# Optimization experiments

Hardware: AMD Instinct MI355X
Metric: run time of the kernel (lower is better)

The kernel has to match this reference:

```python
import jax, jax.numpy as jnp
import numpy as np

B, N, C, H, I, ID = 4, 1024, 1024, 16, 77, 768
HD = C // H
HID = 4 * C


def _ln(t, w, b):
    m = jnp.mean(t, axis=-1, keepdims=True)
    v = jnp.mean((t - m) ** 2, axis=-1, keepdims=True)
    return (t - m) * jax.lax.rsqrt(v + 1e-5) * w + b


def _gelu(t):
    return jax.nn.gelu(t, approximate=False)


def setup_inputs() -> dict:
    key = jax.random.key(0)
    ks = iter(jax.random.split(key, 16))

    def nrm(shape, s=0.02):
        return jax.random.normal(next(ks), shape, jnp.float32) * s

    return {
        'x': jax.random.normal(next(ks), (B, N, C), jnp.float32),
        'instruct_states': jax.random.normal(next(ks), (B, I, ID), jnp.float32),
        'norm1_w': jnp.ones((C,), jnp.float32), 'norm1_b': jnp.zeros((C,), jnp.float32),
        'qkv_w': nrm((3 * C, C)),
        'q_bias': jnp.zeros((C,), jnp.float32), 'v_bias': jnp.zeros((C,), jnp.float32),
        'proj_w': nrm((C, C)), 'proj_b': jnp.zeros((C,), jnp.float32),
        'gamma_1': jnp.full((C,), 1e-5, jnp.float32), 'gamma_2': jnp.full((C,), 1e-5, jnp.float32),
        'norm2_w': jnp.ones((C,), jnp.float32), 'norm2_b': jnp.zeros((C,), jnp.float32),
        'fc1_w': nrm((HID, C)), 'fc1_b': jnp.zeros((HID,), jnp.float32),
        'fc2_w': nrm((C, HID)), 'fc2_b': jnp.zeros((C,), jnp.float32),
        'pfc1_w': nrm((HID, C)), 'pfc1_b': jnp.zeros((HID,), jnp.float32),
        'pfc2_w': nrm((C, HID)), 'pfc2_b': jnp.zeros((C,), jnp.float32),
        'parallel_gate': jnp.full((1,), 0.1, jnp.float32),
        'ir_ln_w': jnp.ones((ID,), jnp.float32), 'ir_ln_b': jnp.zeros((ID,), jnp.float32),
        'ir_l1_w': nrm((C, ID)), 'ir_l1_b': jnp.zeros((C,), jnp.float32),
        'ir_l2_w': nrm((C, C)), 'ir_l2_b': jnp.zeros((C,), jnp.float32),
    }


def reference(x, instruct_states, norm1_w, norm1_b, qkv_w, q_bias, v_bias,
              proj_w, proj_b, gamma_1, gamma_2, norm2_w, norm2_b,
              fc1_w, fc1_b, fc2_w, fc2_b, pfc1_w, pfc1_b, pfc2_w, pfc2_b,
              parallel_gate, ir_ln_w, ir_ln_b, ir_l1_w, ir_l1_b, ir_l2_w, ir_l2_b):
    # instruct_dim_reduce: LN -> Linear -> GELU -> Linear
    kv = _ln(instruct_states, ir_ln_w, ir_ln_b)
    kv = _gelu(kv @ ir_l1_w.T + ir_l1_b) @ ir_l2_w.T + ir_l2_b  # [B, I, C]

    xn = _ln(x, norm1_w, norm1_b)                               # [B, N, C]
    cat = jnp.concatenate([kv, xn], axis=1)                     # [B, I+N, C]
    S = I + N

    qkv_bias = jnp.concatenate([q_bias, jnp.zeros_like(v_bias), v_bias])
    qkv = (cat @ qkv_w.T + qkv_bias).reshape(B, S, 3, H, HD)
    q = qkv[:, :, 0].transpose(0, 2, 1, 3)                      # [B, H, S, HD]
    k = qkv[:, :, 1].transpose(0, 2, 1, 3)
    v = qkv[:, :, 2].transpose(0, 2, 1, 3)

    # only visual queries, keys/values over instructions + visual tokens
    q = q[:, :, I:, :] * (HD ** -0.5)                           # [B, H, N, HD]
    attn = jnp.einsum('bhqd,bhkd->bhqk', q, k)                  # [B, H, N, S]
    attn = jax.nn.softmax(attn, axis=-1)
    o = jnp.einsum('bhqk,bhkd->bqhd', attn, v).reshape(B, N, C)
    o = o @ proj_w.T + proj_b

    x = x + gamma_1 * o                                         # LayerScale residual

    y = _ln(x, norm2_w, norm2_b)
    mlp = _gelu(y @ fc1_w.T + fc1_b) @ fc2_w.T + fc2_b
    pmlp = _gelu(y @ pfc1_w.T + pfc1_b) @ pfc2_w.T + pfc2_b
    x = x + gamma_2 * mlp + parallel_gate * pmlp
    return x
```

## Files before the change

kernel.cpp:

```cpp
#include <hip/hip_runtime.h>
#include <cstdint>

#define Bv   4
#define Nv   1024
#define Cv   1024
#define Hv   16
#define Iv   77
#define IDv  768
#define HDv  64
#define HIDv 4096
#define Sv   (Iv + Nv)
#define BIv  (Bv * Iv)
#define BSv  (Bv * Sv)
#define BNv  (Bv * Nv)
#define SPADv 1152

typedef __bf16 bf16x8_t __attribute__((ext_vector_type(8)));
typedef float  f32x4_t  __attribute__((ext_vector_type(4)));
typedef unsigned short us8_t __attribute__((ext_vector_type(8)));
typedef long  l2_t  __attribute__((ext_vector_type(2)));
typedef int   i32x4_t __attribute__((ext_vector_type(4)));
typedef int   i32x8_t __attribute__((ext_vector_type(8)));

__device__ inline f32x4_t zero4() { f32x4_t z; z[0]=0.f; z[1]=0.f; z[2]=0.f; z[3]=0.f; return z; }

__device__ inline unsigned short f2bf(float f) {
    unsigned int u = __builtin_bit_cast(unsigned int, f);
    u = (u + 0x7fffu + ((u >> 16) & 1u)) >> 16;
    return (unsigned short)u;
}
__device__ inline float bf2f(unsigned short u) {
    return __builtin_bit_cast(float, ((unsigned int)u) << 16);
}
__device__ inline unsigned int f4_fp8(float a, float b, float c, float d) {
    int v = __builtin_amdgcn_cvt_pk_fp8_f32(a, b, 0, false);
    v = __builtin_amdgcn_cvt_pk_fp8_f32(c, d, v, true);
    return (unsigned int)v;
}

__device__ inline float gelu_f(float x) {
    float u = 0.7978845608f * x * (1.0f + 0.044715f * x * x);
    float e = __expf(2.0f * u);
    float t = 1.0f - 2.0f / (e + 1.0f);
    return 0.5f * x * (1.0f + t);
}

__device__ inline void gload_lds16(const void* g, void* l) {
    __builtin_amdgcn_global_load_lds(
        (__attribute__((address_space(1))) void*)(unsigned long long)g,
        (__attribute__((address_space(3))) void*)(unsigned long long)l,
        16, 0, 0);
}

__device__ inline i32x8_t frag32(const unsigned char* p0, const unsigned char* p1) {
    i32x4_t lo = *(const i32x4_t*)p0;
    i32x4_t hi = *(const i32x4_t*)p1;
    i32x8_t r;
    r[0] = lo[0]; r[1] = lo[1]; r[2] = lo[2]; r[3] = lo[3];
    r[4] = hi[0]; r[5] = hi[1]; r[6] = hi[2]; r[7] = hi[3];
    return r;
}

#define PIPE_WAIT(N) do { \
    asm volatile("s_waitcnt vmcnt(" #N ")" ::: "memory"); \
    __builtin_amdgcn_s_barrier(); \
    __builtin_amdgcn_sched_barrier(0); \
} while (0)
#define PIPE_RELEASE() do { \
    __builtin_amdgcn_sched_barrier(0); \
    __builtin_amdgcn_s_barrier(); \
} while (0)

__global__ __launch_bounds__(256) void cvt8_kernel(
        const float* s0, const float* s1, const float* s2, const float* s3,
        const float* s4, const float* s5, const float* s6, const float* s7,
        void* d0, void* d1, void* d2, void* d3,
        void* d4, void* d5, void* d6, void* d7,
        const float* g1, const float* g2, const float* gate) {
    (void)g1;
    long i = (long)blockIdx.x * 256 + threadIdx.x;
    const float* src; void* dst; long off;
    const float* sptr = nullptr; int K4 = 1; float wmul = 1.0f; bool f8 = false;
    if (i < 2097152) {
        if (i < 786432)       { src = s0; dst = d0; off = i; f8 = true; wmul = 32.f; }
        else if (i < 1048576) { src = s1; dst = d1; off = i - 786432;  f8 = true; wmul = 32.f; }
        else                  { src = s2; dst = d2; off = i - 1048576; f8 = true; wmul = 32.f; }
    } else if (i < 4194304) {
        if (i < 3145728)      { src = s3; dst = d3; off = i - 2097152; f8 = true; wmul = 32.f; sptr = g2; K4 = 1024; }
        else                  { src = s4; dst = d4; off = i - 3145728; f8 = true; wmul = 32.f; }
    } else {
        if (i < 5242880)      { src = s5; dst = d5; off = i - 4194304; f8 = true; wmul = 32.f; sptr = gate; K4 = 0x7fffffff; }
        else if (i < 5439488) { src = s6; dst = d6; off = i - 5242880; }
        else                  { src = s7; dst = d7; off = i - 5439488; }
    }
    float sc = (sptr ? sptr[(int)(off / K4)] : 1.0f) * wmul;
    float4 v = ((const float4*)src)[off];
    if (f8) {
        ((unsigned int*)dst)[off] = f4_fp8(v.x * sc, v.y * sc, v.z * sc, v.w * sc);
    } else {
        ushort4 o = {f2bf(v.x * sc), f2bf(v.y * sc), f2bf(v.z * sc), f2bf(v.w * sc)};
        ((ushort4*)dst)[off] = o;
    }
}

__global__ __launch_bounds__(256) void bias_prep_kernel(
        const float* __restrict__ qb, const float* __restrict__ vb,
        const float* __restrict__ fc2b, const float* __restrict__ pfc2b,
        const float* __restrict__ projb_in,
        const float* __restrict__ fc1b, const float* __restrict__ pfc1b,
        const float* __restrict__ g1, const float* __restrict__ g2,
        const float* __restrict__ gate,
        float* __restrict__ qkvb, float* __restrict__ bfuse,
        float* __restrict__ projb, float* __restrict__ bcat) {
    int i = blockIdx.x * 256 + threadIdx.x;
    if (i < 3 * Cv) {
        float v = 0.f;
        if (i < Cv) v = qb[i];
        else if (i >= 2 * Cv) v = vb[i - 2 * Cv];
        qkvb[i] = v;
    } else if (i < 4 * Cv) {
        int n = i - 3 * Cv;
        bfuse[n] = g2[n] * fc2b[n] + gate[0] * pfc2b[n];
    } else if (i < 5 * Cv) {
        int n = i - 4 * Cv;
        projb[n] = g1[n] * projb_in[n];
    } else if (i < 13 * Cv) {
        int j = i - 5 * Cv;
        bcat[j] = (j < HIDv) ? fc1b[j] : pfc1b[j - HIDv];
    }
}

template <int F8>
__global__ __launch_bounds__(256) void ln_kernel(const float* __restrict__ in,
                                                 const float* __restrict__ w,
                                                 const float* __restrict__ bvec,
                                                 void* __restrict__ out,
                                                 int cols, float invcols,
                                                 int div_, int stride_, int off_) {
    const int r = blockIdx.x;
    const int tid = threadIdx.x;
    const float* row = in + (size_t)r * cols;
    float s = 0.f, s2 = 0.f;
    for (int c = tid * 4; c < cols; c += 1024) {
        float4 v = *(const float4*)(row + c);
        s  += v.x + v.y + v.z + v.w;
        s2 += v.x * v.x + v.y * v.y + v.z * v.z + v.w * v.w;
    }
#pragma unroll
    for (int o2 = 32; o2 > 0; o2 >>= 1) { s += __shfl_down(s, o2); s2 += __shfl_down(s2, o2); }
    __shared__ float sh[10];
    const int lane = tid & 63, wave = tid >> 6;
    if (lane == 0) { sh[wave] = s; sh[4 + wave] = s2; }
    __syncthreads();
    if (tid == 0) {
        float S1 = sh[0] + sh[1] + sh[2] + sh[3];
        float S2 = sh[4] + sh[5] + sh[6] + sh[7];
        float mean = S1 * invcols;
        float var  = S2 * invcols - mean * mean;
        sh[8] = mean;
        sh[9] = rsqrtf(var + 1e-5f);
    }
    __syncthreads();
    const float mean = sh[8], rstd = sh[9];
    const size_t orow = (size_t)((r / div_) * stride_ + (r % div_) + off_) * cols;
    for (int c = tid * 4; c < cols; c += 1024) {
        float4 v  = *(const float4*)(row + c);
        float4 wv = *(const float4*)(w + c);
        float4 bv = *(const float4*)(bvec + c);
        float o0 = (v.x - mean) * rstd * wv.x + bv.x;
        float o1 = (v.y - mean) * rstd * wv.y + bv.y;
        float o2 = (v.z - mean) * rstd * wv.z + bv.z;
        float o3 = (v.w - mean) * rstd * wv.w + bv.w;
        if constexpr (F8) {
            *(unsigned int*)((unsigned char*)out + orow + c) =
                f4_fp8(o0 * 16.f, o1 * 16.f, o2 * 16.f, o3 * 16.f);
        } else {
            ushort4 o = {f2bf(o0), f2bf(o1), f2bf(o2), f2bf(o3)};
            *(ushort4*)((unsigned short*)out + orow + c) = o;
        }
    }
}

__global__ __launch_bounds__(256) void proj_ln2_kernel(
        const unsigned short* __restrict__ parts,
        const float* __restrict__ x,
        const float* __restrict__ projb,
        const float* __restrict__ g1,
        const float* __restrict__ w, const float* __restrict__ bvec,
        float* __restrict__ x1, unsigned char* __restrict__ y8) {
    const int r = blockIdx.x;
    const int tid = threadIdx.x;
    const int c = tid * 4;
    const size_t base = (size_t)r * Cv + c;
    float4 xv = *(const float4*)(x + base);
    float4 pb = *(const float4*)(projb + c);
    float4 gv = *(const float4*)(g1 + c);
    ushort4 u0 = *(const ushort4*)(parts + base);
    ushort4 u1 = *(const ushort4*)(parts + (size_t)BNv * Cv + base);
    float4 v;
    v.x = xv.x + pb.x + gv.x * (bf2f(u0.x) + bf2f(u1.x));
    v.y = xv.y + pb.y + gv.y * (bf2f(u0.y) + bf2f(u1.y));
    v.z = xv.z + pb.z + gv.z * (bf2f(u0.z) + bf2f(u1.z));
    v.w = xv.w + pb.w + gv.w * (bf2f(u0.w) + bf2f(u1.w));
    *(float4*)(x1 + base) = v;

    float s  = v.x + v.y + v.z + v.w;
    float s2 = v.x * v.x + v.y * v.y + v.z * v.z + v.w * v.w;
#pragma unroll
    for (int o2 = 32; o2 > 0; o2 >>= 1) { s += __shfl_down(s, o2); s2 += __shfl_down(s2, o2); }
    __shared__ float sh[10];
    const int lane = tid & 63, wave = tid >> 6;
    if (lane == 0) { sh[wave] = s; sh[4 + wave] = s2; }
    __syncthreads();
    if (tid == 0) {
        float S1 = sh[0] + sh[1] + sh[2] + sh[3];
        float S2 = sh[4] + sh[5] + sh[6] + sh[7];
        float mean = S1 * (1.0f / Cv);
        float var  = S2 * (1.0f / Cv) - mean * mean;
        sh[8] = mean;
        sh[9] = rsqrtf(var + 1e-5f);
    }
    __syncthreads();
    const float mean = sh[8], rstd = sh[9];
    float4 wv = *(const float4*)(w + c);
    float4 bv = *(const float4*)(bvec + c);
    float o0 = (v.x - mean) * rstd * wv.x + bv.x;
    float o1 = (v.y - mean) * rstd * wv.y + bv.y;
    float o2 = (v.z - mean) * rstd * wv.z + bv.z;
    float o3 = (v.w - mean) * rstd * wv.w + bv.w;
    *(unsigned int*)(y8 + base) = f4_fp8(o0 * 16.f, o1 * 16.f, o2 * 16.f, o3 * 16.f);
}

template <int MODE>
__global__ __launch_bounds__(256) void gemm_bf16_kernel(
        const unsigned short* __restrict__ A,
        const unsigned short* __restrict__ W,
        const float* __restrict__ bias,
        unsigned short* __restrict__ outp,
        int M, int N, int K) {
    __shared__ unsigned short As[2][128 * 32];
    __shared__ unsigned short Bs[2][128 * 32];
    const int tid  = threadIdx.x;
    const int lane = tid & 63;
    const int wave = tid >> 6;
    const int m16  = lane & 15;
    const int g4   = lane >> 4;
    const int n0 = blockIdx.x * 128;
    const int m0 = blockIdx.y * 128;
    const int wm = (wave >> 1) * 64;
    const int wn = (wave & 1) * 64;

    const int r0  = tid >> 2;
    const int cc0 = (tid & 3) * 8;
    int am0 = m0 + r0;       if (am0 > M - 1) am0 = M - 1;
    int am1 = m0 + r0 + 64;  if (am1 > M - 1) am1 = M - 1;
    const unsigned short* agp0 = A + (size_t)am0 * K + cc0;
    const unsigned short* agp1 = A + (size_t)am1 * K + cc0;
    const unsigned short* bgp0 = W + (size_t)(n0 + r0) * K + cc0;
    const unsigned short* bgp1 = W + (size_t)(n0 + r0 + 64) * K + cc0;

    f32x4_t acc[4][4];
#pragma unroll
    for (int a = 0; a < 4; ++a)
#pragma unroll
        for (int bb = 0; bb < 4; ++bb) acc[a][bb] = zero4();

    auto stage = [&](int buf) {
        gload_lds16(agp0, &As[buf][wave * 512]);
        gload_lds16(agp1, &As[buf][2048 + wave * 512]);
        gload_lds16(bgp0, &Bs[buf][wave * 512]);
        gload_lds16(bgp1, &Bs[buf][2048 + wave * 512]);
        agp0 += 32; agp1 += 32; bgp0 += 32; bgp1 += 32;
    };

    auto body = [&](int cur) {
        bf16x8_t xf[4], wf[4];
#pragma unroll
        for (int bb = 0; bb < 4; ++bb)
            xf[bb] = *(const bf16x8_t*)&As[cur][(wm + bb * 16 + m16) * 32 + g4 * 8];
#pragma unroll
        for (int a = 0; a < 4; ++a)
            wf[a] = *(const bf16x8_t*)&Bs[cur][(wn + a * 16 + m16) * 32 + g4 * 8];
#pragma unroll
        for (int a = 0; a < 4; ++a)
#pragma unroll
            for (int bb = 0; bb < 4; ++bb)
                acc[a][bb] = __builtin_amdgcn_mfma_f32_16x16x32_bf16(wf[a], xf[bb], acc[a][bb], 0, 0, 0);
    };

    const int NIT = K >> 5;
    stage(0);
    stage(1);
    for (int it = 0; it < NIT - 1; ++it) {
        const int cur = it & 1;
        PIPE_WAIT(4);
        body(cur);
        PIPE_RELEASE();
        if (it + 2 < NIT) stage(cur);
    }
    PIPE_WAIT(0);
    body((NIT - 1) & 1);

#pragma unroll
    for (int a = 0; a < 4; ++a) {
        const int cb = n0 + wn + a * 16 + g4 * 4;
        const float4 bv4 = *(const float4*)(bias + cb);
#pragma unroll
        for (int bb = 0; bb < 4; ++bb) {
            const int r = m0 + wm + bb * 16 + m16;
            if (r < M) {
                const float v0 = acc[a][bb][0] + bv4.x;
                const float v1 = acc[a][bb][1] + bv4.y;
                const float v2 = acc[a][bb][2] + bv4.z;
                const float v3 = acc[a][bb][3] + bv4.w;
                if constexpr (MODE == 0) {
                    const size_t idx = (size_t)r * N + cb;
                    ushort4 o = {f2bf(v0), f2bf(v1), f2bf(v2), f2bf(v3)};
                    *(ushort4*)(outp + idx) = o;
                } else if constexpr (MODE == 1) {
                    const size_t idx = (size_t)r * N + cb;
                    ushort4 o = {f2bf(gelu_f(v0)), f2bf(gelu_f(v1)),
                                 f2bf(gelu_f(v2)), f2bf(gelu_f(v3))};
                    *(ushort4*)(outp + idx) = o;
                } else {
                    const int rr2 = (r / Iv) * Sv + (r % Iv);
                    *(unsigned int*)((unsigned char*)outp + (size_t)rr2 * Cv + cb) =
                        f4_fp8(v0 * 16.f, v1 * 16.f, v2 * 16.f, v3 * 16.f);
                }
            }
        }
    }
}

__global__ __launch_bounds__(256) void gemm_fp8_bf16out_kernel(
        const unsigned char* __restrict__ A,
        const unsigned char* __restrict__ W,
        const float* __restrict__ bias,
        unsigned short* __restrict__ outp,
        int M, int N, int K) {
    __shared__ unsigned char As[2][128 * 128];
    __shared__ unsigned char Bs[2][128 * 128];
    const int tid  = threadIdx.x;
    const int lane = tid & 63;
    const int wave = tid >> 6;
    const int m16  = lane & 15;
    const int g4   = lane >> 4;
    const int n0 = blockIdx.x * 128;
    const int m0 = blockIdx.y * 128;
    const int wm = (wave >> 1) * 64;
    const int wn = (wave & 1) * 64;

    const int rowin = tid >> 3;
    const int sslot = (tid & 7) ^ (rowin & 7);
    const unsigned char* agp[4];
#pragma unroll
    for (int j = 0; j < 4; ++j) {
        int gr = m0 + j * 32 + rowin; if (gr > M - 1) gr = M - 1;
        agp[j] = A + (size_t)gr * K + sslot * 16;
    }
    const unsigned char* bgp = W + (size_t)(n0 + rowin) * K + sslot * 16;

    const int sw = m16 & 7;
    const int ra0 = ((2 * g4) ^ sw) * 16;
    const int ra1 = ((2 * g4 + 1) ^ sw) * 16;

    f32x4_t acc[4][4];
#pragma unroll
    for (int a = 0; a < 4; ++a)
#pragma unroll
        for (int bb = 0; bb < 4; ++bb) acc[a][bb] = zero4();

    auto stage = [&](int buf) {
#pragma unroll
        for (int j = 0; j < 4; ++j) {
            gload_lds16(agp[j], &As[buf][j * 4096 + wave * 1024]);
            gload_lds16(bgp + (size_t)j * 32 * K, &Bs[buf][j * 4096 + wave * 1024]);
            agp[j] += 128;
        }
        bgp += 128;
    };

    stage(0);
    const int NIT = K >> 7;
    for (int it = 0; it < NIT; ++it) {
        const int cur = it & 1;
        __syncthreads();
        if (it + 1 < NIT) stage(cur ^ 1);
        i32x8_t xv[4], wv[4];
#pragma unroll
        for (int bb = 0; bb < 4; ++bb) {
            const unsigned char* rb = &As[cur][(wm + bb * 16 + m16) * 128];
            xv[bb] = frag32(rb + ra0, rb + ra1);
        }
#pragma unroll
        for (int a = 0; a < 4; ++a) {
            const unsigned char* rb = &Bs[cur][(wn + a * 16 + m16) * 128];
            wv[a] = frag32(rb + ra0, rb + ra1);
        }
#pragma unroll
        for (int a = 0; a < 4; ++a)
#pragma unroll
            for (int bb = 0; bb < 4; ++bb)
                acc[a][bb] = __builtin_amdgcn_mfma_scale_f32_16x16x128_f8f6f4(
                    wv[a], xv[bb], acc[a][bb], 0, 0, 0, 0x7f7f7f7f, 0, 0x7f7f7f7f);
    }

    const float ds = 1.0f / 512.0f;
#pragma unroll
    for (int a = 0; a < 4; ++a) {
        const int cb = n0 + wn + a * 16 + g4 * 4;
        const float4 bv4 = *(const float4*)(bias + cb);
#pragma unroll
        for (int bb = 0; bb < 4; ++bb) {
            const int r = m0 + wm + bb * 16 + m16;
            if (r < M) {
                const size_t idx = (size_t)r * N + cb;
                ushort4 o = {f2bf(acc[a][bb][0] * ds + bv4.x),
                             f2bf(acc[a][bb][1] * ds + bv4.y),
                             f2bf(acc[a][bb][2] * ds + bv4.z),
                             f2bf(acc[a][bb][3] * ds + bv4.w)};
                *(ushort4*)(outp + idx) = o;
            }
        }
    }
}

__global__ __launch_bounds__(256) void gemm_fp8_gelu_kernel(
        const unsigned char* __restrict__ A,
        const unsigned char* __restrict__ W,
        const float* __restrict__ bias,
        unsigned char* __restrict__ outp,
        int M, int N, int K) {
    __shared__ unsigned char As[2][128 * 128];
    __shared__ unsigned char Bs[2][128 * 128];
    const int tid  = threadIdx.x;
    const int lane = tid & 63;
    const int wave = tid >> 6;
    const int m16  = lane & 15;
    const int g4   = lane >> 4;
    const int bid = blockIdx.x;
    const int xcd = bid & 7, l = bid >> 3;
    const int by = (xcd << 2) | (l & 3);
    const int bx = l >> 2;
    const int n0 = bx * 128;
    const int m0 = by * 128;
    const int wm = (wave >> 1) * 64;
    const int wn = (wave & 1) * 64;

    const int rowin = tid >> 3;
    const int sslot = (tid & 7) ^ (rowin & 7);
    const unsigned char* agp = A + (size_t)(m0 + rowin) * K + sslot * 16;
    const unsigned char* bgp = W + (size_t)(n0 + rowin) * K + sslot * 16;

    const int sw = m16 & 7;
    const int ra0 = ((2 * g4) ^ sw) * 16;
    const int ra1 = ((2 * g4 + 1) ^ sw) * 16;

    f32x4_t acc[4][4];
#pragma unroll
    for (int a = 0; a < 4; ++a)
#pragma unroll
        for (int bb = 0; bb < 4; ++bb) acc[a][bb] = zero4();

    auto stage = [&](int buf) {
#pragma unroll
        for (int j = 0; j < 4; ++j) {
            gload_lds16(agp + (size_t)j * 32 * K, &As[buf][j * 4096 + wave * 1024]);
            gload_lds16(bgp + (size_t)j * 32 * K, &Bs[buf][j * 4096 + wave * 1024]);
        }
        agp += 128; bgp += 128;
    };

    stage(0);
    const int NIT = K >> 7;
    for (int it = 0; it < NIT; ++it) {
        const int cur = it & 1;
        __syncthreads();
        if (it + 1 < NIT) stage(cur ^ 1);
        i32x8_t xv[4], wv[4];
#pragma unroll
        for (int bb = 0; bb < 4; ++bb) {
            const unsigned char* rb = &As[cur][(wm + bb * 16 + m16) * 128];
            xv[bb] = frag32(rb + ra0, rb + ra1);
        }
#pragma unroll
        for (int a = 0; a < 4; ++a) {
            const unsigned char* rb = &Bs[cur][(wn + a * 16 + m16) * 128];
            wv[a] = frag32(rb + ra0, rb + ra1);
        }
#pragma unroll
        for (int a = 0; a < 4; ++a)
#pragma unroll
            for (int bb = 0; bb < 4; ++bb)
                acc[a][bb] = __builtin_amdgcn_mfma_scale_f32_16x16x128_f8f6f4(
                    wv[a], xv[bb], acc[a][bb], 0, 0, 0, 0x7f7f7f7f, 0, 0x7f7f7f7f);
    }

    const float ds = 1.0f / 512.0f;
#pragma unroll
    for (int a = 0; a < 4; ++a) {
        const int cb = n0 + wn + a * 16 + g4 * 4;
        const float4 bv4 = *(const float4*)(bias + cb);
#pragma unroll
        for (int bb = 0; bb < 4; ++bb) {
            const int r = m0 + wm + bb * 16 + m16;
            const size_t idx = (size_t)r * N + cb;
            unsigned int pk = f4_fp8(gelu_f(acc[a][bb][0] * ds + bv4.x) * 16.f,
                                     gelu_f(acc[a][bb][1] * ds + bv4.y) * 16.f,
                                     gelu_f(acc[a][bb][2] * ds + bv4.z) * 16.f,
                                     gelu_f(acc[a][bb][3] * ds + bv4.w) * 16.f);
            *(unsigned int*)(outp + idx) = pk;
        }
    }
}

__global__ __launch_bounds__(256) void gemm_fp8_splitk_kernel(
        const unsigned char* __restrict__ A1,
        const unsigned char* __restrict__ W1,
        const unsigned char* __restrict__ A2,
        const unsigned char* __restrict__ W2,
        unsigned short* __restrict__ parts,
        int M, int N, int lda, int ldw, int Kc, int zsplit) {
    __shared__ unsigned char As[2][128 * 128];
    __shared__ unsigned char Bs[2][128 * 128];
    const int tid  = threadIdx.x;
    const int lane = tid & 63;
    const int wave = tid >> 6;
    const int m16  = lane & 15;
    const int g4   = lane >> 4;
    const int bid = blockIdx.x;
    const int xcd = bid & 7, l = bid >> 3;
    const int by = (xcd << 2) | (l & 3);
    const int rr = l >> 2;
    const int bx = rr & 7;
    const int z  = rr >> 3;
    const int n0 = bx * 128;
    const int m0 = by * 128;
    const int wm = (wave >> 1) * 64;
    const int wn = (wave & 1) * 64;

    const unsigned char* A = (z < zsplit) ? A1 : A2;
    const unsigned char* W = (z < zsplit) ? W1 : W2;
    const int k0 = (z % zsplit) * Kc;

    const int rowin = tid >> 3;
    const int sslot = (tid & 7) ^ (rowin & 7);
    const unsigned char* agp = A + (size_t)(m0 + rowin) * lda + k0 + sslot * 16;
    const unsigned char* bgp = W + (size_t)(n0 + rowin) * ldw + k0 + sslot * 16;

    const int sw = m16 & 7;
    const int ra0 = ((2 * g4) ^ sw) * 16;
    const int ra1 = ((2 * g4 + 1) ^ sw) * 16;

    f32x4_t acc[4][4];
#pragma unroll
    for (int a = 0; a < 4; ++a)
#pragma unroll
        for (int bb = 0; bb < 4; ++bb) acc[a][bb] = zero4();

    auto stage = [&](int buf) {
#pragma unroll
        for (int j = 0; j < 4; ++j) {
            gload_lds16(agp + (size_t)j * 32 * lda, &As[buf][j * 4096 + wave * 1024]);
            gload_lds16(bgp + (size_t)j * 32 * ldw, &Bs[buf][j * 4096 + wave * 1024]);
        }
        agp += 128; bgp += 128;
    };

    stage(0);
    const int NIT = Kc >> 7;
    for (int it = 0; it < NIT; ++it) {
        const int cur = it & 1;
        __syncthreads();
        if (it + 1 < NIT) stage(cur ^ 1);
        i32x8_t xv[4], wv[4];
#pragma unroll
        for (int bb = 0; bb < 4; ++bb) {
            const unsigned char* rb = &As[cur][(wm + bb * 16 + m16) * 128];
            xv[bb] = frag32(rb + ra0, rb + ra1);
        }
#pragma unroll
        for (int a = 0; a < 4; ++a) {
            const unsigned char* rb = &Bs[cur][(wn + a * 16 + m16) * 128];
            wv[a] = frag32(rb + ra0, rb + ra1);
        }
#pragma unroll
        for (int a = 0; a < 4; ++a)
#pragma unroll
            for (int bb = 0; bb < 4; ++bb)
                acc[a][bb] = __builtin_amdgcn_mfma_scale_f32_16x16x128_f8f6f4(
                    wv[a], xv[bb], acc[a][bb], 0, 0, 0, 0x7f7f7f7f, 0, 0x7f7f7f7f);
    }

    unsigned short* pz = parts + (size_t)z * M * N;
    const float ds = 1.0f / 512.0f;
#pragma unroll
    for (int a = 0; a < 4; ++a) {
        const int cb = n0 + wn + a * 16 + g4 * 4;
#pragma unroll
        for (int bb = 0; bb < 4; ++bb) {
            const int r = m0 + wm + bb * 16 + m16;
            const size_t idx = (size_t)r * N + cb;
            ushort4 o = {f2bf(acc[a][bb][0] * ds), f2bf(acc[a][bb][1] * ds),
                         f2bf(acc[a][bb][2] * ds), f2bf(acc[a][bb][3] * ds)};
            *(ushort4*)(pz + idx) = o;
        }
    }
}

template <int NP>
__global__ __launch_bounds__(256) void reduce_kernel(
        const unsigned short* __restrict__ parts,
        const float* __restrict__ resid,
        const float* __restrict__ bias,
        float* __restrict__ out, int MN, int N4mask) {
    int i = blockIdx.x * 256 + threadIdx.x;
    if (i * 4 >= MN) return;
    float4 res = ((const float4*)resid)[i];
    float4 bv  = *(const float4*)(bias + (i & N4mask) * 4);
    float4 o = {res.x + bv.x, res.y + bv.y, res.z + bv.z, res.w + bv.w};
#pragma unroll
    for (int z = 0; z < NP; ++z) {
        ushort4 u = ((const ushort4*)(parts + (size_t)z * MN))[i];
        o.x += bf2f(u.x); o.y += bf2f(u.y); o.z += bf2f(u.z); o.w += bf2f(u.w);
    }
    ((float4*)out)[i] = o;
}

__global__ __launch_bounds__(256) void vtrans_kernel(const unsigned short* __restrict__ qkv,
                                                     unsigned short* __restrict__ vt) {
    __shared__ unsigned short Vs[64 * 64];
    const int stile = blockIdx.x;
    const int bh = blockIdx.y;
    const int b = bh >> 4, h = bh & 15;
    const int tid = threadIdx.x;
#pragma unroll
    for (int j = 0; j < 2; ++j) {
        int c = j * 256 + tid;
        int r = c >> 3, d8 = (c & 7) * 8;
        int s = stile * 64 + r;
        uint4 v = {0u, 0u, 0u, 0u};
        if (s < Sv) v = *(const uint4*)(qkv + ((size_t)(b * Sv + s) * 3 + 2) * Cv + h * 64 + d8);
        *(uint4*)&Vs[r * 64 + d8] = v;
    }
    __syncthreads();
    const int d  = tid >> 2;
    const int p0 = (tid & 3) * 16;
    unsigned short tmp[16];
#pragma unroll
    for (int e = 0; e < 16; ++e) {
        int p = p0 + e;
        int s_local = (p & 32) + 16 * ((p >> 2) & 1) + 4 * ((p & 31) >> 3) + (p & 3);
        tmp[e] = Vs[s_local * 64 + d];
    }
    unsigned short* dst = vt + ((size_t)bh * 64 + d) * SPADv + stile * 64 + p0;
    *(uint4*)dst       = *(const uint4*)&tmp[0];
    *(uint4*)(dst + 8) = *(const uint4*)&tmp[8];
}

__global__ __launch_bounds__(256) void attn_kernel(const unsigned short* __restrict__ qkv,
                                                   const unsigned short* __restrict__ vt,
                                                   unsigned char* __restrict__ o) {
    __shared__ unsigned short Qs[64 * 64];
    __shared__ unsigned short Ks[2][64 * 64];
    __shared__ unsigned short Vts[2][64 * 64];

    const int tid  = threadIdx.x;
    const int lane = tid & 63;
    const int wave = tid >> 6;
    const int m16  = lane & 15;
    const int g4   = lane >> 4;
    const int qt = blockIdx.x;
    const int bh = blockIdx.y;
    const int b = bh >> 4, h = bh & 15;

    const int lr = lane >> 3;
    const int csw = ((lane & 7) ^ lr) * 8;
    const int sw7 = m16 & 7;

#pragma unroll
    for (int j = 0; j < 2; ++j) {
        int r = wave * 16 + j * 8 + lr;
        int s = Iv + qt * 64 + r;
        gload_lds16(qkv + ((size_t)(b * Sv + s) * 3) * Cv + h * 64 + csw,
                    &Qs[(wave * 16 + j * 8) * 64]);
    }

    auto stage_kv = [&](int st, int buf) {
#pragma unroll
        for (int j = 0; j < 2; ++j) {
            int r = wave * 16 + j * 8 + lr;
            int s = st * 64 + r; if (s > Sv - 1) s = Sv - 1;
            gload_lds16(qkv + ((size_t)(b * Sv + s) * 3 + 1) * Cv + h * 64 + csw,
                        &Ks[buf][(wave * 16 + j * 8) * 64]);
            gload_lds16(vt + ((size_t)bh * 64 + r) * SPADv + st * 64 + csw,
                        &Vts[buf][(wave * 16 + j * 8) * 64]);
        }
    };

    f32x4_t oacc[4];
#pragma unroll
    for (int dt = 0; dt < 4; ++dt) oacc[dt] = zero4();
    float m_run = -1e30f, l_run = 0.f;

    stage_kv(0, 0);
    __syncthreads();

    const bf16x8_t qf0 = *(const bf16x8_t*)&Qs[(wave * 16 + m16) * 64 + ((g4 ^ sw7) * 8)];
    const bf16x8_t qf1 = *(const bf16x8_t*)&Qs[(wave * 16 + m16) * 64 + (((4 + g4) ^ sw7) * 8)];

    const int NT = (Sv + 63) / 64;
    for (int st = 0; st < NT; ++st) {
        const int cur = st & 1;
        if (st + 1 < NT) stage_kv(st + 1, cur ^ 1);

        f32x4_t sc[4];
#pragma unroll
        for (int kt = 0; kt < 4; ++kt) {
            bf16x8_t k0 = *(const bf16x8_t*)&Ks[cur][(kt * 16 + m16) * 64 + ((g4 ^ sw7) * 8)];
            bf16x8_t k1 = *(const bf16x8_t*)&Ks[cur][(kt * 16 + m16) * 64 + (((4 + g4) ^ sw7) * 8)];
            f32x4_t z = zero4();
            z = __builtin_amdgcn_mfma_f32_16x16x32_bf16(k0, qf0, z, 0, 0, 0);
            z = __builtin_amdgcn_mfma_f32_16x16x32_bf16(k1, qf1, z, 0, 0, 0);
            sc[kt] = z;
        }

        float mx = -1e30f;
#pragma unroll
        for (int kt = 0; kt < 4; ++kt)
#pragma unroll
            for (int r = 0; r < 4; ++r) {
                int key = st * 64 + kt * 16 + g4 * 4 + r;
                float v = sc[kt][r] * 0.125f;
                v = (key < Sv) ? v : -1e30f;
                sc[kt][r] = v;
                mx = fmaxf(mx, v);
            }
        mx = fmaxf(mx, __shfl_xor(mx, 16));
        mx = fmaxf(mx, __shfl_xor(mx, 32));
        const float mnew  = fmaxf(m_run, mx);
        const float alpha = __expf(m_run - mnew);
        m_run = mnew;
        float sum = 0.f;
#pragma unroll
        for (int kt = 0; kt < 4; ++kt)
#pragma unroll
            for (int r = 0; r < 4; ++r) {
                float p = __expf(sc[kt][r] - mnew);
                sc[kt][r] = p;
                sum += p;
            }
        sum += __shfl_xor(sum, 16);
        sum += __shfl_xor(sum, 32);
        l_run = l_run * alpha + sum;
#pragma unroll
        for (int dt = 0; dt < 4; ++dt) oacc[dt] *= alpha;

        us8_t pu0, pu1;
#pragma unroll
        for (int j = 0; j < 8; ++j) {
            pu0[j] = f2bf(sc[(j >> 2)][j & 3]);
            pu1[j] = f2bf(sc[2 + (j >> 2)][j & 3]);
        }
        const bf16x8_t pf0 = __builtin_bit_cast(bf16x8_t, pu0);
        const bf16x8_t pf1 = __builtin_bit_cast(bf16x8_t, pu1);

#pragma unroll
        for (int dt = 0; dt < 4; ++dt) {
            bf16x8_t v0 = *(const bf16x8_t*)&Vts[cur][(dt * 16 + m16) * 64 + ((g4 ^ sw7) * 8)];
            bf16x8_t v1 = *(const bf16x8_t*)&Vts[cur][(dt * 16 + m16) * 64 + (((4 + g4) ^ sw7) * 8)];
            oacc[dt] = __builtin_amdgcn_mfma_f32_16x16x32_bf16(v0, pf0, oacc[dt], 0, 0, 0);
            oacc[dt] = __builtin_amdgcn_mfma_f32_16x16x32_bf16(v1, pf1, oacc[dt], 0, 0, 0);
        }
        __syncthreads();
    }

    const float inv16 = 16.0f / l_run;
    const int q = qt * 64 + wave * 16 + m16;
    const size_t row = (size_t)(b * Nv + q) * Cv + h * 64;
#pragma unroll
    for (int dt = 0; dt < 4; ++dt) {
        *(unsigned int*)&o[row + dt * 16 + g4 * 4] =
            f4_fp8(oacc[dt][0] * inv16, oacc[dt][1] * inv16,
                   oacc[dt][2] * inv16, oacc[dt][3] * inv16);
    }
}

extern "C" void kernel_launch(void* const* d_in, const int* in_sizes, int n_in,
                              void* d_out, int out_size, void* d_ws, size_t ws_size,
                              hipStream_t stream) {
    (void)in_sizes; (void)n_in; (void)out_size; (void)ws_size;
    const float* x       = (const float*)d_in[0];
    const float* instr   = (const float*)d_in[1];
    const float* norm1_w = (const float*)d_in[2];
    const float* norm1_b = (const float*)d_in[3];
    const float* qkv_w   = (const float*)d_in[4];
    const float* q_bias  = (const float*)d_in[5];
    const float* v_bias  = (const float*)d_in[6];
    const float* proj_w  = (const float*)d_in[7];
    const float* proj_b  = (const float*)d_in[8];
    const float* gamma_1 = (const float*)d_in[9];
    const float* gamma_2 = (const float*)d_in[10];
    const float* norm2_w = (const float*)d_in[11];
    const float* norm2_b = (const float*)d_in[12];
    const float* fc1_w   = (const float*)d_in[13];
    const float* fc1_b   = (const float*)d_in[14];
    const float* fc2_w   = (const float*)d_in[15];
    const float* fc2_b   = (const float*)d_in[16];
    const float* pfc1_w  = (const float*)d_in[17];
    const float* pfc1_b  = (const float*)d_in[18];
    const float* pfc2_w  = (const float*)d_in[19];
    const float* pfc2_b  = (const float*)d_in[20];
    const float* gate    = (const float*)d_in[21];
    const float* ir_ln_w = (const float*)d_in[22];
    const float* ir_ln_b = (const float*)d_in[23];
    const float* ir_l1_w = (const float*)d_in[24];
    const float* ir_l1_b = (const float*)d_in[25];
    const float* ir_l2_w = (const float*)d_in[26];
    const float* ir_l2_b = (const float*)d_in[27];
    float* out = (float*)d_out;

    char* ws = (char*)d_ws;
    size_t off = 0;
    auto alloc = [&](size_t bytes) -> char* {
        char* p = ws + off;
        off += (bytes + 255) & ~(size_t)255;
        return p;
    };
    unsigned char*  w_qkv8 = (unsigned char*)alloc((size_t)3 * Cv * Cv);
    unsigned char*  w_proj8= (unsigned char*)alloc((size_t)Cv * Cv);
    unsigned char*  w_mlp1 = (unsigned char*)alloc((size_t)2 * HIDv * Cv);
    unsigned char*  w_fc2  = (unsigned char*)alloc((size_t)Cv * HIDv);
    unsigned char*  w_pfc2 = (unsigned char*)alloc((size_t)Cv * HIDv);
    unsigned short* w_ir1  = (unsigned short*)alloc((size_t)Cv * IDv * 2);
    unsigned short* w_ir2  = (unsigned short*)alloc((size_t)Cv * Cv * 2);
    float*          qkvb   = (float*)alloc((size_t)3 * Cv * 4);
    float*          bfuse  = (float*)alloc((size_t)Cv * 4);
    float*          projb  = (float*)alloc((size_t)Cv * 4);
    float*          bcat   = (float*)alloc((size_t)2 * HIDv * 4);
    unsigned short* irln   = (unsigned short*)alloc((size_t)BIv * IDv * 2);
    unsigned short* h1     = (unsigned short*)alloc((size_t)BIv * Cv * 2);
    unsigned char*  cat8   = (unsigned char*)alloc((size_t)BSv * Cv);
    unsigned short* qkvbuf = (unsigned short*)alloc((size_t)BSv * 3 * Cv * 2);
    unsigned char*  obuf8  = (unsigned char*)alloc((size_t)BNv * Cv);
    float*          x1     = (float*)alloc((size_t)BNv * Cv * 4);
    unsigned char*  ybuf8  = (unsigned char*)alloc((size_t)BNv * Cv);
    unsigned char*  gbufA  = (unsigned char*)alloc((size_t)BNv * 2 * HIDv);
    unsigned short* fpart  = (unsigned short*)alloc((size_t)2 * BNv * Cv * 2);
    unsigned short* vt     = (unsigned short*)gbufA;
    unsigned short* ppart  = fpart;

    cvt8_kernel<<<22272, 256, 0, stream>>>(qkv_w, proj_w, fc1_w, fc2_w, pfc1_w, pfc2_w,
                                           ir_l1_w, ir_l2_w,
                                           w_qkv8, w_proj8, w_mlp1, w_fc2,
                                           w_mlp1 + (size_t)HIDv * Cv, w_pfc2,
                                           w_ir1, w_ir2,
                                           gamma_1, gamma_2, gate);

    bias_prep_kernel<<<52, 256, 0, stream>>>(q_bias, v_bias, fc2_b, pfc2_b, proj_b,
                                             fc1_b, pfc1_b,
                                             gamma_1, gamma_2, gate,
                                             qkvb, bfuse, projb, bcat);

    ln_kernel<0><<<BIv, 256, 0, stream>>>(instr, ir_ln_w, ir_ln_b, irln,
                                          IDv, 1.0f / IDv, 1 << 28, 0, 0);
    ln_kernel<1><<<BNv, 256, 0, stream>>>(x, norm1_w, norm1_b, cat8,
                                          Cv, 1.0f / Cv, Nv, Sv, Iv);
    gemm_bf16_kernel<1><<<dim3(Cv / 128, (BIv + 127) / 128), 256, 0, stream>>>(
        irln, w_ir1, ir_l1_b, h1, BIv, Cv, IDv);
    gemm_bf16_kernel<2><<<dim3(Cv / 128, (BIv + 127) / 128), 256, 0, stream>>>(
        h1, w_ir2, ir_l2_b, (unsigned short*)cat8, BIv, Cv, Cv);

    gemm_fp8_bf16out_kernel<<<dim3(3 * Cv / 128, (BSv + 127) / 128), 256, 0, stream>>>(
        cat8, w_qkv8, qkvb, qkvbuf, BSv, 3 * Cv, Cv);

    vtrans_kernel<<<dim3(18, Bv * Hv), 256, 0, stream>>>(qkvbuf, vt);
    attn_kernel<<<dim3(Nv / 64, Bv * Hv), 256, 0, stream>>>(qkvbuf, vt, obuf8);

    gemm_fp8_splitk_kernel<<<512, 256, 0, stream>>>(
        obuf8, w_proj8, obuf8, w_proj8, ppart,
        BNv, Cv, Cv, Cv, Cv / 2, 2);
    proj_ln2_kernel<<<BNv, 256, 0, stream>>>(
        ppart, x, projb, gamma_1, norm2_w, norm2_b, x1, ybuf8);

    gemm_fp8_gelu_kernel<<<2048, 256, 0, stream>>>(
        ybuf8, w_mlp1, bcat, gbufA, BNv, 2 * HIDv, Cv);

    gemm_fp8_splitk_kernel<<<512, 256, 0, stream>>>(
        gbufA, w_fc2, gbufA + HIDv, w_pfc2, fpart,
        BNv, Cv, 2 * HIDv, HIDv, HIDv, 1);
    reduce_kernel<2><<<(BNv * Cv / 4 + 255) / 256, 256, 0, stream>>>(
        fpart, x1, bfuse, out, BNv * Cv, Cv / 4 - 1);
}
```

Measured before the change: 438.7 us.

## Replace instruct-reduce GEMMs with per-wave tiny tiles; raise MFMA priority in attention

The two small instruction-reduction GEMMs (M=308) now use a kernel where each wave computes a 16x64 tile, loading operands straight from global memory with no LDS staging or barriers. This gives far more blocks than the old 128x128 tiling, which launched only 24 blocks, so it is meant to spread the small problem across more CUs. The trade is no data reuse through shared memory. Separately, the attention kernel raises wave priority around its MFMA sections with s_setprio, to interleave compute better with the softmax and loads of other waves.

```diff
diff --git a/kernel.cpp b/kernel.cpp
--- a/kernel.cpp
+++ b/kernel.cpp
@@ -60,16 +60,6 @@
     r[4] = hi[0]; r[5] = hi[1]; r[6] = hi[2]; r[7] = hi[3];
     return r;
 }
-
-#define PIPE_WAIT(N) do { \
-    asm volatile("s_waitcnt vmcnt(" #N ")" ::: "memory"); \
-    __builtin_amdgcn_s_barrier(); \
-    __builtin_amdgcn_sched_barrier(0); \
-} while (0)
-#define PIPE_RELEASE() do { \
-    __builtin_amdgcn_sched_barrier(0); \
-    __builtin_amdgcn_s_barrier(); \
-} while (0)
 
 __global__ __launch_bounds__(256) void cvt8_kernel(
         const float* s0, const float* s1, const float* s2, const float* s3,
@@ -232,102 +222,59 @@
 }
 
 template <int MODE>
-__global__ __launch_bounds__(256) void gemm_bf16_kernel(
+__global__ __launch_bounds__(256) void gemm_tiny_kernel(
         const unsigned short* __restrict__ A,
         const unsigned short* __restrict__ W,
         const float* __restrict__ bias,
         unsigned short* __restrict__ outp,
         int M, int N, int K) {
-    __shared__ unsigned short As[2][128 * 32];
-    __shared__ unsigned short Bs[2][128 * 32];
-    const int tid  = threadIdx.x;
-    const int lane = tid & 63;
-    const int wave = tid >> 6;
+    const int lane = threadIdx.x & 63;
+    const int wave = threadIdx.x >> 6;
     const int m16  = lane & 15;
     const int g4   = lane >> 4;
-    const int n0 = blockIdx.x * 128;
-    const int m0 = blockIdx.y * 128;
-    const int wm = (wave >> 1) * 64;
-    const int wn = (wave & 1) * 64;
-
-    const int r0  = tid >> 2;
-    const int cc0 = (tid & 3) * 8;
-    int am0 = m0 + r0;       if (am0 > M - 1) am0 = M - 1;
-    int am1 = m0 + r0 + 64;  if (am1 > M - 1) am1 = M - 1;
-    const unsigned short* agp0 = A + (size_t)am0 * K + cc0;
-    const unsigned short* agp1 = A + (size_t)am1 * K + cc0;
-    const unsigned short* bgp0 = W + (size_t)(n0 + r0) * K + cc0;
-    const unsigned short* bgp1 = W + (size_t)(n0 + r0 + 64) * K + cc0;
-
-    f32x4_t acc[4][4];
-#pragma unroll
-    for (int a = 0; a < 4; ++a)
-#pragma unroll
-        for (int bb = 0; bb < 4; ++bb) acc[a][bb] = zero4();
-
-    auto stage = [&](int buf) {
-        gload_lds16(agp0, &As[buf][wave * 512]);
-        gload_lds16(agp1, &As[buf][2048 + wave * 512]);
-        gload_lds16(bgp0, &Bs[buf][wave * 512]);
-        gload_lds16(bgp1, &Bs[buf][2048 + wave * 512]);
-        agp0 += 32; agp1 += 32; bgp0 += 32; bgp1 += 32;
-    };
-
-    auto body = [&](int cur) {
-        bf16x8_t xf[4], wf[4];
-#pragma unroll
-        for (int bb = 0; bb < 4; ++bb)
-            xf[bb] = *(const bf16x8_t*)&As[cur][(wm + bb * 16 + m16) * 32 + g4 * 8];
-#pragma unroll
-        for (int a = 0; a < 4; ++a)
-            wf[a] = *(const bf16x8_t*)&Bs[cur][(wn + a * 16 + m16) * 32 + g4 * 8];
-#pragma unroll
-        for (int a = 0; a < 4; ++a)
-#pragma unroll
-            for (int bb = 0; bb < 4; ++bb)
-                acc[a][bb] = __builtin_amdgcn_mfma_f32_16x16x32_bf16(wf[a], xf[bb], acc[a][bb], 0, 0, 0);
-    };
-
-    const int NIT = K >> 5;
-    stage(0);
-    stage(1);
-    for (int it = 0; it < NIT - 1; ++it) {
-        const int cur = it & 1;
-        PIPE_WAIT(4);
-        body(cur);
-        PIPE_RELEASE();
-        if (it + 2 < NIT) stage(cur);
-    }
-    PIPE_WAIT(0);
-    body((NIT - 1) & 1);
-
+    const int wid  = blockIdx.x * 4 + wave;
+    const int ntiles = N >> 6;
+    const int mti = wid / ntiles;
+    if (mti * 16 >= M + 15) return;
+    const int m0 = mti * 16;
+    const int n0 = (wid % ntiles) * 64;
+
+    int am = m0 + m16; if (am > M - 1) am = M - 1;
+    const unsigned short* ap = A + (size_t)am * K + g4 * 8;
+    const unsigned short* wp = W + (size_t)(n0 + m16) * K + g4 * 8;
+
+    f32x4_t acc[4];
+#pragma unroll
+    for (int a = 0; a < 4; ++a) acc[a] = zero4();
+
+#pragma unroll 2
+    for (int kk = 0; kk < K; kk += 32) {
+        bf16x8_t xf = *(const bf16x8_t*)(ap + kk);
+#pragma unroll
+        for (int a = 0; a < 4; ++a) {
+            bf16x8_t wf = *(const bf16x8_t*)(wp + (size_t)a * 16 * K + kk);
+            acc[a] = __builtin_amdgcn_mfma_f32_16x16x32_bf16(wf, xf, acc[a], 0, 0, 0);
+        }
+    }
+
+    const int r = m0 + m16;
+    if (r >= M) return;
 #pragma unroll
     for (int a = 0; a < 4; ++a) {
-        const int cb = n0 + wn + a * 16 + g4 * 4;
+        const int cb = n0 + a * 16 + g4 * 4;
         const float4 bv4 = *(const float4*)(bias + cb);
-#pragma unroll
-        for (int bb = 0; bb < 4; ++bb) {
-            const int r = m0 + wm + bb * 16 + m16;
-            if (r < M) {
-                const float v0 = acc[a][bb][0] + bv4.x;
-                const float v1 = acc[a][bb][1] + bv4.y;
-                const float v2 = acc[a][bb][2] + bv4.z;
-                const float v3 = acc[a][bb][3] + bv4.w;
-                if constexpr (MODE == 0) {
-                    const size_t idx = (size_t)r * N + cb;
-                    ushort4 o = {f2bf(v0), f2bf(v1), f2bf(v2), f2bf(v3)};
-                    *(ushort4*)(outp + idx) = o;
-                } else if constexpr (MODE == 1) {
-                    const size_t idx = (size_t)r * N + cb;
-                    ushort4 o = {f2bf(gelu_f(v0)), f2bf(gelu_f(v1)),
-                                 f2bf(gelu_f(v2)), f2bf(gelu_f(v3))};
-                    *(ushort4*)(outp + idx) = o;
-                } else {
-                    const int rr2 = (r / Iv) * Sv + (r % Iv);
-                    *(unsigned int*)((unsigned char*)outp + (size_t)rr2 * Cv + cb) =
-                        f4_fp8(v0 * 16.f, v1 * 16.f, v2 * 16.f, v3 * 16.f);
-                }
-            }
+        const float v0 = acc[a][0] + bv4.x;
+        const float v1 = acc[a][1] + bv4.y;
+        const float v2 = acc[a][2] + bv4.z;
+        const float v3 = acc[a][3] + bv4.w;
+        if constexpr (MODE == 1) {
+            ushort4 o = {f2bf(gelu_f(v0)), f2bf(gelu_f(v1)),
+                         f2bf(gelu_f(v2)), f2bf(gelu_f(v3))};
+            *(ushort4*)(outp + (size_t)r * N + cb) = o;
+        } else {
+            const int rr2 = (r / Iv) * Sv + (r % Iv);
+            *(unsigned int*)((unsigned char*)outp + (size_t)rr2 * Cv + cb) =
+                f4_fp8(v0 * 16.f, v1 * 16.f, v2 * 16.f, v3 * 16.f);
         }
     }
 }
@@ -715,6 +662,7 @@
         if (st + 1 < NT) stage_kv(st + 1, cur ^ 1);
 
         f32x4_t sc[4];
+        __builtin_amdgcn_s_setprio(1);
 #pragma unroll
         for (int kt = 0; kt < 4; ++kt) {
             bf16x8_t k0 = *(const bf16x8_t*)&Ks[cur][(kt * 16 + m16) * 64 + ((g4 ^ sw7) * 8)];
@@ -724,6 +672,7 @@
             z = __builtin_amdgcn_mfma_f32_16x16x32_bf16(k1, qf1, z, 0, 0, 0);
             sc[kt] = z;
         }
+        __builtin_amdgcn_s_setprio(0);
 
         float mx = -1e30f;
 #pragma unroll
@@ -765,6 +714,7 @@
         const bf16x8_t pf0 = __builtin_bit_cast(bf16x8_t, pu0);
         const bf16x8_t pf1 = __builtin_bit_cast(bf16x8_t, pu1);
 
+        __builtin_amdgcn_s_setprio(1);
 #pragma unroll
         for (int dt = 0; dt < 4; ++dt) {
             bf16x8_t v0 = *(const bf16x8_t*)&Vts[cur][(dt * 16 + m16) * 64 + ((g4 ^ sw7) * 8)];
@@ -772,6 +722,7 @@
             oacc[dt] = __builtin_amdgcn_mfma_f32_16x16x32_bf16(v0, pf0, oacc[dt], 0, 0, 0);
             oacc[dt] = __builtin_amdgcn_mfma_f32_16x16x32_bf16(v1, pf1, oacc[dt], 0, 0, 0);
         }
+        __builtin_amdgcn_s_setprio(0);
         __syncthreads();
     }
 
@@ -866,10 +817,13 @@
                                           IDv, 1.0f / IDv, 1 << 28, 0, 0);
     ln_kernel<1><<<BNv, 256, 0, stream>>>(x, norm1_w, norm1_b, cat8,
                                           Cv, 1.0f / Cv, Nv, Sv, Iv);
-    gemm_bf16_kernel<1><<<dim3(Cv / 128, (BIv + 127) / 128), 256, 0, stream>>>(
-        irln, w_ir1, ir_l1_b, h1, BIv, Cv, IDv);
-    gemm_bf16_kernel<2><<<dim3(Cv / 128, (BIv + 127) / 128), 256, 0, stream>>>(
-        h1, w_ir2, ir_l2_b, (unsigned short*)cat8, BIv, Cv, Cv);
+    {
+        const int wtiles = ((BIv + 15) / 16) * (Cv / 64);
+        gemm_tiny_kernel<1><<<(wtiles + 3) / 4, 256, 0, stream>>>(
+            irln, w_ir1, ir_l1_b, h1, BIv, Cv, IDv);
+        gemm_tiny_kernel<2><<<(wtiles + 3) / 4, 256, 0, stream>>>(
+            h1, w_ir2, ir_l2_b, (unsigned short*)cat8, BIv, Cv, Cv);
+    }
 
     gemm_fp8_bf16out_kernel<<<dim3(3 * Cv / 128, (BSv + 127) / 128), 256, 0, stream>>>(
         cat8, w_qkv8, qkvb, qkvbuf, BSv, 3 * Cv, Cv);
```

New measurement: 453.6 us. 3.4% more time.

## Process two query groups per wave in attention to reuse staged K/V

Applied to the files above, without the earlier changes.

The attention kernel now handles 128 queries per block, with each wave owning two 16-query groups that keep separate online-softmax state and share the same K/V fragments loaded from LDS. Q fragments are read straight from global memory into registers, so the Q shared-memory buffer is gone. Each K/V tile staged into LDS now feeds twice as many queries, roughly halving K/V global and LDS traffic per query. In exchange the grid is halved to 512 blocks, and register pressure rises from the doubled accumulators and the preloaded K/V fragments, which may lower occupancy.

```diff
diff --git a/kernel.cpp b/kernel.cpp
--- a/kernel.cpp
+++ b/kernel.cpp
@@ -661,7 +661,6 @@
 __global__ __launch_bounds__(256) void attn_kernel(const unsigned short* __restrict__ qkv,
                                                    const unsigned short* __restrict__ vt,
                                                    unsigned char* __restrict__ o) {
-    __shared__ unsigned short Qs[64 * 64];
     __shared__ unsigned short Ks[2][64 * 64];
     __shared__ unsigned short Vts[2][64 * 64];
 
@@ -678,12 +677,13 @@
     const int csw = ((lane & 7) ^ lr) * 8;
     const int sw7 = m16 & 7;
 
-#pragma unroll
-    for (int j = 0; j < 2; ++j) {
-        int r = wave * 16 + j * 8 + lr;
-        int s = Iv + qt * 64 + r;
-        gload_lds16(qkv + ((size_t)(b * Sv + s) * 3) * Cv + h * 64 + csw,
-                    &Qs[(wave * 16 + j * 8) * 64]);
+    bf16x8_t qf0[2], qf1[2];
+#pragma unroll
+    for (int g = 0; g < 2; ++g) {
+        const int s = Iv + qt * 128 + wave * 32 + g * 16 + m16;
+        const unsigned short* qp = qkv + ((size_t)(b * Sv + s) * 3) * Cv + h * 64 + g4 * 8;
+        qf0[g] = *(const bf16x8_t*)qp;
+        qf1[g] = *(const bf16x8_t*)(qp + 32);
     }
 
     auto stage_kv = [&](int st, int buf) {
@@ -698,91 +698,113 @@
         }
     };
 
-    f32x4_t oacc[4];
-#pragma unroll
-    for (int dt = 0; dt < 4; ++dt) oacc[dt] = zero4();
-    float m_run = -1e30f, l_run = 0.f;
+    f32x4_t oaccA[4], oaccB[4];
+#pragma unroll
+    for (int dt = 0; dt < 4; ++dt) { oaccA[dt] = zero4(); oaccB[dt] = zero4(); }
+    float m_runA = -1e30f, l_runA = 0.f;
+    float m_runB = -1e30f, l_runB = 0.f;
 
     stage_kv(0, 0);
     __syncthreads();
-
-    const bf16x8_t qf0 = *(const bf16x8_t*)&Qs[(wave * 16 + m16) * 64 + ((g4 ^ sw7) * 8)];
-    const bf16x8_t qf1 = *(const bf16x8_t*)&Qs[(wave * 16 + m16) * 64 + (((4 + g4) ^ sw7) * 8)];
 
     const int NT = (Sv + 63) / 64;
     for (int st = 0; st < NT; ++st) {
         const int cur = st & 1;
         if (st + 1 < NT) stage_kv(st + 1, cur ^ 1);
 
-        f32x4_t sc[4];
+        bf16x8_t k0[4], k1[4];
 #pragma unroll
         for (int kt = 0; kt < 4; ++kt) {
-            bf16x8_t k0 = *(const bf16x8_t*)&Ks[cur][(kt * 16 + m16) * 64 + ((g4 ^ sw7) * 8)];
-            bf16x8_t k1 = *(const bf16x8_t*)&Ks[cur][(kt * 16 + m16) * 64 + (((4 + g4) ^ sw7) * 8)];
-            f32x4_t z = zero4();
-            z = __builtin_amdgcn_mfma_f32_16x16x32_bf16(k0, qf0, z, 0, 0, 0);
-            z = __builtin_amdgcn_mfma_f32_16x16x32_bf16(k1, qf1, z, 0, 0, 0);
-            sc[kt] = z;
-        }
-
-        float mx = -1e30f;
-#pragma unroll
-        for (int kt = 0; kt < 4; ++kt)
-#pragma unroll
-            for (int r = 0; r < 4; ++r) {
-                int key = st * 64 + kt * 16 + g4 * 4 + r;
-                float v = sc[kt][r] * 0.125f;
-                v = (key < Sv) ? v : -1e30f;
-                sc[kt][r] = v;
-                mx = fmaxf(mx, v);
+            k0[kt] = *(const bf16x8_t*)&Ks[cur][(kt * 16 + m16) * 64 + ((g4 ^ sw7) * 8)];
+            k1[kt] = *(const bf16x8_t*)&Ks[cur][(kt * 16 + m16) * 64 + (((4 + g4) ^ sw7) * 8)];
+        }
+        bf16x8_t v0[4], v1[4];
+#pragma unroll
+        for (int dt = 0; dt < 4; ++dt) {
+            v0[dt] = *(const bf16x8_t*)&Vts[cur][(dt * 16 + m16) * 64 + ((g4 ^ sw7) * 8)];
+            v1[dt] = *(const bf16x8_t*)&Vts[cur][(dt * 16 + m16) * 64 + (((4 + g4) ^ sw7) * 8)];
+        }
+
+#pragma unroll
+        for (int g = 0; g < 2; ++g) {
+            const bf16x8_t qa = g ? qf0[1] : qf0[0];
+            const bf16x8_t qb = g ? qf1[1] : qf1[0];
+            f32x4_t* oacc = g ? oaccB : oaccA;
+            float m_run = g ? m_runB : m_runA;
+            float l_run = g ? l_runB : l_runA;
+
+            f32x4_t sc[4];
+#pragma unroll
+            for (int kt = 0; kt < 4; ++kt) {
+                f32x4_t z = zero4();
+                z = __builtin_amdgcn_mfma_f32_16x16x32_bf16(k0[kt], qa, z, 0, 0, 0);
+                z = __builtin_amdgcn_mfma_f32_16x16x32_bf16(k1[kt], qb, z, 0, 0, 0);
+                sc[kt] = z;
             }
-        mx = fmaxf(mx, __shfl_xor(mx, 16));
-        mx = fmaxf(mx, __shfl_xor(mx, 32));
-        const float mnew  = fmaxf(m_run, mx);
-        const float alpha = __expf(m_run - mnew);
-        m_run = mnew;
-        float sum = 0.f;
-#pragma unroll
-        for (int kt = 0; kt < 4; ++kt)
-#pragma unroll
-            for (int r = 0; r < 4; ++r) {
-                float p = __expf(sc[kt][r] - mnew);
-                sc[kt][r] = p;
-                sum += p;
+
+            float mx = -1e30f;
+#pragma unroll
+            for (int kt = 0; kt < 4; ++kt)
+#pragma unroll
+                for (int r = 0; r < 4; ++r) {
+                    int key = st * 64 + kt * 16 + g4 * 4 + r;
+                    float v = sc[kt][r] * 0.125f;
+                    v = (key < Sv) ? v : -1e30f;
+                    sc[kt][r] = v;
+                    mx = fmaxf(mx, v);
+                }
+            mx = fmaxf(mx, __shfl_xor(mx, 16));
+            mx = fmaxf(mx, __shfl_xor(mx, 32));
+            const float mnew  = fmaxf(m_run, mx);
+            const float alpha = __expf(m_run - mnew);
+            m_run = mnew;
+            float sum = 0.f;
+#pragma unroll
+            for (int kt = 0; kt < 4; ++kt)
+#pragma unroll
+                for (int r = 0; r < 4; ++r) {
+                    float p = __expf(sc[kt][r] - mnew);
+                    sc[kt][r] = p;
+                    sum += p;
+                }
+            sum += __shfl_xor(sum, 16);
+            sum += __shfl_xor(sum, 32);
+            l_run = l_run * alpha + sum;
+#pragma unroll
+            for (int dt = 0; dt < 4; ++dt) oacc[dt] *= alpha;
+
+            us8_t pu0, pu1;
+#pragma unroll
+            for (int j = 0; j < 8; ++j) {
+                pu0[j] = f2bf(sc[(j >> 2)][j & 3]);
+                pu1[j] = f2bf(sc[2 + (j >> 2)][j & 3]);
             }
-        sum += __shfl_xor(sum, 16);
-        sum += __shfl_xor(sum, 32);
-        l_run = l_run * alpha + sum;
-#pragma unroll
-        for (int dt = 0; dt < 4; ++dt) oacc[dt] *= alpha;
-
-        us8_t pu0, pu1;
-#pragma unroll
-        for (int j = 0; j < 8; ++j) {
-            pu0[j] = f2bf(sc[(j >> 2)][j & 3]);
-            pu1[j] = f2bf(sc[2 + (j >> 2)][j & 3]);
-        }
-        const bf16x8_t pf0 = __builtin_bit_cast(bf16x8_t, pu0);
-        const bf16x8_t pf1 = __builtin_bit_cast(bf16x8_t, pu1);
-
+            const bf16x8_t pf0 = __builtin_bit_cast(bf16x8_t, pu0);
+            const bf16x8_t pf1 = __builtin_bit_cast(bf16x8_t, pu1);
+
+#pragma unroll
+            for (int dt = 0; dt < 4; ++dt) {
+                oacc[dt] = __builtin_amdgcn_mfma_f32_16x16x32_bf16(v0[dt], pf0, oacc[dt], 0, 0, 0);
+                oacc[dt] = __builtin_amdgcn_mfma_f32_16x16x32_bf16(v1[dt], pf1, oacc[dt], 0, 0, 0);
+            }
+            if (g) { m_runB = m_run; l_runB = l_run; }
+            else   { m_runA = m_run; l_runA = l_run; }
+        }
+        __syncthreads();
+    }
+
+#pragma unroll
+    for (int g = 0; g < 2; ++g) {
+        const f32x4_t* oacc = g ? oaccB : oaccA;
+        const float inv16 = 16.0f / (g ? l_runB : l_runA);
+        const int q = qt * 128 + wave * 32 + g * 16 + m16;
+        const size_t row = (size_t)(b * Nv + q) * Cv + h * 64;
 #pragma unroll
         for (int dt = 0; dt < 4; ++dt) {
-            bf16x8_t v0 = *(const bf16x8_t*)&Vts[cur][(dt * 16 + m16) * 64 + ((g4 ^ sw7) * 8)];
-            bf16x8_t v1 = *(const bf16x8_t*)&Vts[cur][(dt * 16 + m16) * 64 + (((4 + g4) ^ sw7) * 8)];
-            oacc[dt] = __builtin_amdgcn_mfma_f32_16x16x32_bf16(v0, pf0, oacc[dt], 0, 0, 0);
-            oacc[dt] = __builtin_amdgcn_mfma_f32_16x16x32_bf16(v1, pf1, oacc[dt], 0, 0, 0);
-        }
-        __syncthreads();
-    }
-
-    const float inv16 = 16.0f / l_run;
-    const int q = qt * 64 + wave * 16 + m16;
-    const size_t row = (size_t)(b * Nv + q) * Cv + h * 64;
-#pragma unroll
-    for (int dt = 0; dt < 4; ++dt) {
-        *(unsigned int*)&o[row + dt * 16 + g4 * 4] =
-            f4_fp8(oacc[dt][0] * inv16, oacc[dt][1] * inv16,
-                   oacc[dt][2] * inv16, oacc[dt][3] * inv16);
+            *(unsigned int*)&o[row + dt * 16 + g4 * 4] =
+                f4_fp8(oacc[dt][0] * inv16, oacc[dt][1] * inv16,
+                       oacc[dt][2] * inv16, oacc[dt][3] * inv16);
+        }
     }
 }
 
@@ -875,7 +897,7 @@
         cat8, w_qkv8, qkvb, qkvbuf, BSv, 3 * Cv, Cv);
 
     vtrans_kernel<<<dim3(18, Bv * Hv), 256, 0, stream>>>(qkvbuf, vt);
-    attn_kernel<<<dim3(Nv / 64, Bv * Hv), 256, 0, stream>>>(qkvbuf, vt, obuf8);
+    attn_kernel<<<dim3(Nv / 128, Bv * Hv), 256, 0, stream>>>(qkvbuf, vt, obuf8);
 
     gemm_fp8_splitk_kernel<<<512, 256, 0, stream>>>(
         obuf8, w_proj8, obuf8, w_proj8, ppart,
```

After: 432.2 us. About the same (-1.5%).
